# Kernel optimization log

Hardware: AMD Instinct MI355X
Metric: run time of the kernel (lower is better)

The kernel has to match this reference:

```python
import jax, jax.numpy as jnp
import numpy as np

BATCH, T, D_MODEL, DIM = 8, 4096, 512, 512
R_MIN, R_MAX, MAX_PHASE = 0.0, 1.0, 6.28


def setup_inputs() -> dict:
    key = jax.random.key(0)
    ks = jax.random.split(key, 8)
    x = jax.random.normal(ks[0], (BATCH, T, D_MODEL), dtype=jnp.float32)
    h0 = jnp.zeros((BATCH, 1, DIM), dtype=jnp.float32)
    # nu_log / theta_log per the module's initializers
    u1 = jax.random.uniform(ks[1], (DIM,))
    nu_log = jnp.log(-0.5 * jnp.log(u1 * (R_MAX ** 2 - R_MIN ** 2) + R_MIN ** 2)).astype(jnp.float32)
    u2 = jax.random.uniform(ks[2], (DIM,))
    theta_log = jnp.log(MAX_PHASE * u2).astype(jnp.float32)
    # B ~ N(0,1)/sqrt(2*D_in), C ~ N(0,1)/sqrt(D_out)
    B_re = (jax.random.normal(ks[3], (D_MODEL, DIM)) / jnp.sqrt(2.0 * D_MODEL)).astype(jnp.float32)
    B_im = (jax.random.normal(ks[4], (D_MODEL, DIM)) / jnp.sqrt(2.0 * D_MODEL)).astype(jnp.float32)
    C_re = (jax.random.normal(ks[5], (DIM, D_MODEL)) / jnp.sqrt(float(D_MODEL))).astype(jnp.float32)
    C_im = (jax.random.normal(ks[6], (DIM, D_MODEL)) / jnp.sqrt(float(D_MODEL))).astype(jnp.float32)
    D_param = jax.random.normal(ks[7], (D_MODEL,)).astype(jnp.float32)
    # gamma_log = log(sqrt(1 - |Lambda|^2)) with Lambda from nu/theta
    diag_lambda = jnp.exp(-jnp.exp(nu_log) + 1j * jnp.exp(theta_log))
    gamma_log = jnp.log(jnp.sqrt(1.0 - jnp.abs(diag_lambda) ** 2)).astype(jnp.float32)
    return {"x": x, "h0": h0, "nu_log": nu_log, "theta_log": theta_log,
            "B_re": B_re, "B_im": B_im, "C_re": C_re, "C_im": C_im,
            "D_param": D_param, "gamma_log": gamma_log}


def _binary_op(ei, ej):
    a_i, b_i = ei
    a_j, b_j = ej
    return (a_j * a_i, a_j * b_i + b_j)


def reference(x, h0, nu_log, theta_log, B_re, B_im, C_re, C_im, D_param, gamma_log):
    B, T_len, _ = x.shape
    Lambda = jnp.exp(-jnp.exp(nu_log) + 1j * jnp.exp(theta_log))            # (N,) complex
    B_norm = (B_re + 1j * B_im) * jnp.exp(gamma_log)[None, :]               # (D,N) complex
    C = C_re + 1j * C_im                                                     # (N,D) complex
    # Input projection: Bu[b,t,n] = sum_d x[b,t,d] * B_norm[d,n]
    Bu = jnp.einsum('btd,dn->btn', x.astype(jnp.complex64), B_norm)
    Bu = jnp.concatenate([h0.astype(jnp.complex64), Bu], axis=1)             # (B,T+1,N)
    Lam = jnp.broadcast_to(Lambda, Bu.shape)                                 # (B,T+1,N)
    _, H = jax.lax.associative_scan(_binary_op, (Lam, Bu), axis=1)
    H = H[:, 1:]                                                             # (B,T,N)
    y = jnp.einsum('btn,nd->btd', H, C).real + D_param * x                   # (B,T,D)
    new_h = H[:, -1:]                                                        # (B,1,N) complex
    return (y, new_h)
```

## Files before the change

kernel.cpp:

```cpp
#include <hip/hip_runtime.h>

#define T_LEN 4096
#define DMODEL 512
#define DIM 512
#define NBATCH 8
#define MROWS (NBATCH * T_LEN)
#define NCHUNK 128
#define LCHUNK 32

typedef __attribute__((ext_vector_type(8))) short short8;
typedef __attribute__((ext_vector_type(4))) float float4v;

__device__ __forceinline__ ushort f2b(float f) {
    union { float fl; unsigned u; } v; v.fl = f;
    unsigned u = v.u;
    return (ushort)((u + 0x7FFFu + ((u >> 16) & 1u)) >> 16);
}
__device__ __forceinline__ float b2f(ushort u) {
    union { unsigned u; float f; } v; v.u = (unsigned)u << 16; return v.f;
}

__device__ __forceinline__ void glds16(const ushort* g, ushort* l) {
    __builtin_amdgcn_global_load_lds(
        (const __attribute__((address_space(1))) void*)g,
        (__attribute__((address_space(3))) void*)l, 16, 0, 0);
}


__global__ __launch_bounds__(256) void k_prep_x(const float* __restrict__ x,
                                                ushort* __restrict__ xb) {
    int i = (blockIdx.x * 256 + threadIdx.x) * 4;
    float4 v = *(const float4*)(x + i);
    ushort4 o;
    o.x = f2b(v.x); o.y = f2b(v.y); o.z = f2b(v.z); o.w = f2b(v.w);
    *(ushort4*)(xb + i) = o;
}

__global__ __launch_bounds__(256) void k_prep_B(const float* __restrict__ Bre,
                                                const float* __restrict__ Bim,
                                                const float* __restrict__ gamma_log,
                                                ushort* __restrict__ BT) {
    int idx = blockIdx.x * 256 + threadIdx.x;
    int n = idx >> 9;
    int d = idx & 511;
    float v;
    if (n < 512) v = Bre[d * 512 + n] * __expf(gamma_log[n]);
    else { int nn = n - 512; v = Bim[d * 512 + nn] * __expf(gamma_log[nn]); }
    BT[idx] = f2b(v);
}

__global__ __launch_bounds__(256) void k_prep_C(const float* __restrict__ Cre,
                                                const float* __restrict__ Cim,
                                                ushort* __restrict__ CT) {
    int idx = blockIdx.x * 256 + threadIdx.x;
    int d = idx >> 10;
    int k = idx & 1023;
    float v = (k < 512) ? Cre[k * 512 + d] : -Cim[(k - 512) * 512 + d];
    CT[idx] = f2b(v);
}

template<int K, int MODE>
__global__ __launch_bounds__(256) void k_gemm(
    const ushort* __restrict__ A, const ushort* __restrict__ Bt,
    ushort* __restrict__ oRe, ushort* __restrict__ oIm,
    float* __restrict__ y, const float* __restrict__ x, const float* __restrict__ Dp) {
    __shared__ ushort sA[128 * 32];
    __shared__ ushort sB[128 * 32];
    const int tid = threadIdx.x;
    const int m0 = blockIdx.y * 128;
    const int n0 = blockIdx.x * 128;
    const int wave = tid >> 6;
    const int lane = tid & 63;
    const int wm = (wave >> 1) * 64;
    const int wn = (wave & 1) * 64;
    const int lr = lane & 15;
    const int quad = lane >> 4;

    const int srow = wave * 32 + (lane >> 2);
    const int scol = (lane & 3) * 8;
    const ushort* gA0 = A + (size_t)(m0 + srow) * K + scol;
    const ushort* gB0 = Bt + (size_t)(n0 + srow) * K + scol;
    ushort* lA0 = &sA[(wave * 32) * 32];
    ushort* lA1 = &sA[(wave * 32 + 16) * 32];
    ushort* lB0 = &sB[(wave * 32) * 32];
    ushort* lB1 = &sB[(wave * 32 + 16) * 32];

    float4v acc[4][4];
#pragma unroll
    for (int i = 0; i < 4; i++)
#pragma unroll
        for (int j = 0; j < 4; j++) {
            float4v z = {0.f, 0.f, 0.f, 0.f};
            acc[i][j] = z;
        }

    for (int k0 = 0; k0 < K; k0 += 32) {
        __syncthreads();
        glds16(gA0 + k0, lA0);
        glds16(gA0 + (size_t)16 * K + k0, lA1);
        glds16(gB0 + k0, lB0);
        glds16(gB0 + (size_t)16 * K + k0, lB1);
        __syncthreads();

        short8 af[4], bfr[4];
#pragma unroll
        for (int i = 0; i < 4; i++) af[i] = *(const short8*)&sA[(wm + i * 16 + lr) * 32 + quad * 8];
#pragma unroll
        for (int j = 0; j < 4; j++) bfr[j] = *(const short8*)&sB[(wn + j * 16 + lr) * 32 + quad * 8];
#pragma unroll
        for (int i = 0; i < 4; i++)
#pragma unroll
            for (int j = 0; j < 4; j++)
                acc[i][j] = __builtin_amdgcn_mfma_f32_16x16x32_bf16(af[i], bfr[j], acc[i][j], 0, 0, 0);
    }

#pragma unroll
    for (int i = 0; i < 4; i++) {
#pragma unroll
        for (int j = 0; j < 4; j++) {
            int gmb = m0 + wm + i * 16 + quad * 4;
            int gn = n0 + wn + j * 16 + lr;
#pragma unroll
            for (int r = 0; r < 4; r++) {
                float v = acc[i][j][r];
                int row = gmb + r;
                if (MODE == 1) {
                    if (gn < 512) oRe[(size_t)row * 512 + gn] = f2b(v);
                    else oIm[(size_t)row * 512 + (gn - 512)] = f2b(v);
                } else {
                    size_t o = (size_t)row * 512 + gn;
                    y[o] = v + Dp[gn] * x[o];
                }
            }
        }
    }
}


__device__ __forceinline__ void lambda_of(const float* nu_log, const float* theta_log,
                                          int n, float& lre, float& lim) {
    float e = __expf(nu_log[n]);
    float th = __expf(theta_log[n]);
    float rad = __expf(-e);
    float s, c;
    __sincosf(th, &s, &c);
    lre = rad * c;
    lim = rad * s;
}

__global__ __launch_bounds__(256) void k_scan1(const ushort* __restrict__ BuRe,
                                               const ushort* __restrict__ BuIm,
                                               const float* __restrict__ nu_log,
                                               const float* __restrict__ theta_log,
                                               float* __restrict__ cRe, float* __restrict__ cIm) {
    int n2 = threadIdx.x;
    int b = blockIdx.x >> 7;
    int c = blockIdx.x & 127;
    float lre0, lim0, lre1, lim1;
    lambda_of(nu_log, theta_log, 2 * n2, lre0, lim0);
    lambda_of(nu_log, theta_log, 2 * n2 + 1, lre1, lim1);
    float hr0 = 0.f, hi0 = 0.f, hr1 = 0.f, hi1 = 0.f;
    size_t base = ((size_t)b * T_LEN + (size_t)c * LCHUNK) * 512 + 2 * n2;
#pragma unroll 8
    for (int j = 0; j < LCHUNK; j++) {
        ushort2 ur = *(const ushort2*)(BuRe + base + (size_t)j * 512);
        ushort2 ui = *(const ushort2*)(BuIm + base + (size_t)j * 512);
        float br0 = b2f(ur.x), br1 = b2f(ur.y), bi0 = b2f(ui.x), bi1 = b2f(ui.y);
        float nr0 = lre0 * hr0 - lim0 * hi0 + br0;
        float ni0 = lre0 * hi0 + lim0 * hr0 + bi0;
        hr0 = nr0; hi0 = ni0;
        float nr1 = lre1 * hr1 - lim1 * hi1 + br1;
        float ni1 = lre1 * hi1 + lim1 * hr1 + bi1;
        hr1 = nr1; hi1 = ni1;
    }
    size_t co = ((size_t)b * NCHUNK + c) * 512 + 2 * n2;
    *(float2*)(cRe + co) = make_float2(hr0, hr1);
    *(float2*)(cIm + co) = make_float2(hi0, hi1);
}

__global__ __launch_bounds__(256) void k_scan2(const float* __restrict__ cRe,
                                               const float* __restrict__ cIm,
                                               const float* __restrict__ h0,
                                               const float* __restrict__ nu_log,
                                               const float* __restrict__ theta_log,
                                               float* __restrict__ pRe, float* __restrict__ pIm,
                                               float* __restrict__ newH, int newh_mode) {
    int idx = blockIdx.x * 256 + threadIdx.x;
    int b = idx >> 9;
    int n = idx & 511;
    float lre, lim;
    lambda_of(nu_log, theta_log, n, lre, lim);
    float Lr = lre, Li = lim;
#pragma unroll
    for (int s = 0; s < 5; s++) {
        float nr = Lr * Lr - Li * Li;
        float ni = 2.f * Lr * Li;
        Lr = nr; Li = ni;
    }
    float cr = h0[b * 512 + n];
    float ci = 0.f;
    for (int c = 0; c < NCHUNK; c++) {
        size_t o = ((size_t)b * NCHUNK + c) * 512 + n;
        pRe[o] = cr;
        pIm[o] = ci;
        float ar = cRe[o], ai = cIm[o];
        float nr = Lr * cr - Li * ci + ar;
        float ni = Lr * ci + Li * cr + ai;
        cr = nr; ci = ni;
    }
    size_t ci_idx = (size_t)b * 512 + n;
    if (newh_mode == 1) {
        newH[ci_idx] = cr;
        newH[(size_t)NBATCH * 512 + ci_idx] = ci;
    } else if (newh_mode == 2) {
        newH[ci_idx] = cr;
    } else {
        newH[ci_idx * 2] = cr;
        newH[ci_idx * 2 + 1] = ci;
    }
}

__global__ __launch_bounds__(256) void k_scan3(const ushort* __restrict__ BuRe,
                                               const ushort* __restrict__ BuIm,
                                               const float* __restrict__ pRe,
                                               const float* __restrict__ pIm,
                                               const float* __restrict__ nu_log,
                                               const float* __restrict__ theta_log,
                                               ushort* __restrict__ Hbf) {
    int n2 = threadIdx.x;
    int b = blockIdx.x >> 7;
    int c = blockIdx.x & 127;
    float lre0, lim0, lre1, lim1;
    lambda_of(nu_log, theta_log, 2 * n2, lre0, lim0);
    lambda_of(nu_log, theta_log, 2 * n2 + 1, lre1, lim1);
    size_t co = ((size_t)b * NCHUNK + c) * 512 + 2 * n2;
    float2 frv = *(const float2*)(pRe + co);
    float2 fiv = *(const float2*)(pIm + co);
    float fr0 = frv.x, fr1 = frv.y, fi0 = fiv.x, fi1 = fiv.y;
    float pr0 = lre0, pi0 = lim0, pr1 = lre1, pi1 = lim1;
    float hr0 = 0.f, hi0 = 0.f, hr1 = 0.f, hi1 = 0.f;
    size_t row0 = (size_t)b * T_LEN + (size_t)c * LCHUNK;
#pragma unroll 4
    for (int j = 0; j < LCHUNK; j++) {
        size_t base = (row0 + j) * 512 + 2 * n2;
        ushort2 ur = *(const ushort2*)(BuRe + base);
        ushort2 ui = *(const ushort2*)(BuIm + base);
        float br0 = b2f(ur.x), br1 = b2f(ur.y), bi0 = b2f(ui.x), bi1 = b2f(ui.y);
        float nr0 = lre0 * hr0 - lim0 * hi0 + br0;
        float ni0 = lre0 * hi0 + lim0 * hr0 + bi0;
        hr0 = nr0; hi0 = ni0;
        float nr1 = lre1 * hr1 - lim1 * hi1 + br1;
        float ni1 = lre1 * hi1 + lim1 * hr1 + bi1;
        hr1 = nr1; hi1 = ni1;
        float vr0 = hr0 + pr0 * fr0 - pi0 * fi0;
        float vi0 = hi0 + pr0 * fi0 + pi0 * fr0;
        float vr1 = hr1 + pr1 * fr1 - pi1 * fi1;
        float vi1 = hi1 + pr1 * fi1 + pi1 * fr1;
        size_t hrow = (row0 + j) * 1024;
        ushort2 wre, wim;
        wre.x = f2b(vr0); wre.y = f2b(vr1);
        wim.x = f2b(vi0); wim.y = f2b(vi1);
        *(ushort2*)(Hbf + hrow + 2 * n2) = wre;
        *(ushort2*)(Hbf + hrow + 512 + 2 * n2) = wim;
        float npr0 = pr0 * lre0 - pi0 * lim0;
        float npi0 = pr0 * lim0 + pi0 * lre0;
        pr0 = npr0; pi0 = npi0;
        float npr1 = pr1 * lre1 - pi1 * lim1;
        float npi1 = pr1 * lim1 + pi1 * lre1;
        pr1 = npr1; pi1 = npi1;
    }
}


extern "C" void kernel_launch(void* const* d_in, const int* in_sizes, int n_in,
                              void* d_out, int out_size, void* d_ws, size_t ws_size,
                              hipStream_t stream) {
    const float* x         = (const float*)d_in[0];
    const float* h0        = (const float*)d_in[1];
    const float* nu_log    = (const float*)d_in[2];
    const float* theta_log = (const float*)d_in[3];
    const float* B_re      = (const float*)d_in[4];
    const float* B_im      = (const float*)d_in[5];
    const float* C_re      = (const float*)d_in[6];
    const float* C_im      = (const float*)d_in[7];
    const float* D_param   = (const float*)d_in[8];
    const float* gamma_log = (const float*)d_in[9];

    char* ws = (char*)d_ws;
    size_t off = 0;
    ushort* Xb   = (ushort*)(ws + off); off += (size_t)MROWS * 512 * 2;
    ushort* BT   = (ushort*)(ws + off); off += (size_t)1024 * 512 * 2;
    ushort* CT   = (ushort*)(ws + off); off += (size_t)512 * 1024 * 2;
    ushort* BuRe = (ushort*)(ws + off); off += (size_t)MROWS * 512 * 2;
    ushort* BuIm = (ushort*)(ws + off); off += (size_t)MROWS * 512 * 2;
    ushort* Hbf  = (ushort*)(ws + off); off += (size_t)MROWS * 1024 * 2;
    float*  cRe  = (float*)(ws + off); off += (size_t)NBATCH * NCHUNK * 512 * 4;
    float*  cIm  = (float*)(ws + off); off += (size_t)NBATCH * NCHUNK * 512 * 4;
    float*  pRe  = (float*)(ws + off); off += (size_t)NBATCH * NCHUNK * 512 * 4;
    float*  pIm  = (float*)(ws + off); off += (size_t)NBATCH * NCHUNK * 512 * 4;

    float* y_out = (float*)d_out;
    float* newH  = (float*)d_out + (size_t)MROWS * 512;

    const int tail = out_size - MROWS * 512;
    int newh_mode = 0;
    if (tail == NBATCH * 512 * 2) newh_mode = 1;
    else if (tail == NBATCH * 512) newh_mode = 2;

    k_prep_x<<<dim3(MROWS * 512 / 4 / 256), dim3(256), 0, stream>>>(x, Xb);
    k_prep_B<<<dim3(1024 * 512 / 256), dim3(256), 0, stream>>>(B_re, B_im, gamma_log, BT);
    k_prep_C<<<dim3(512 * 1024 / 256), dim3(256), 0, stream>>>(C_re, C_im, CT);

    k_gemm<512, 1><<<dim3(1024 / 128, MROWS / 128), dim3(256), 0, stream>>>(
        Xb, BT, BuRe, BuIm, nullptr, nullptr, nullptr);

    k_scan1<<<dim3(NBATCH * NCHUNK), dim3(256), 0, stream>>>(BuRe, BuIm, nu_log, theta_log, cRe, cIm);
    k_scan2<<<dim3(NBATCH * 512 / 256), dim3(256), 0, stream>>>(cRe, cIm, h0, nu_log, theta_log, pRe, pIm, newH, newh_mode);
    k_scan3<<<dim3(NBATCH * NCHUNK), dim3(256), 0, stream>>>(BuRe, BuIm, pRe, pIm, nu_log, theta_log, Hbf);

    k_gemm<1024, 2><<<dim3(512 / 128, MROWS / 128), dim3(256), 0, stream>>>(
        Hbf, CT, nullptr, nullptr, y_out, x, D_param);
}
```

Baseline: 315.9 us.

## Deepen GEMM K tile with XOR-swizzled LDS, XCD-aware block mapping, smaller scan2 blocks

Both GEMMs now stage a 64-wide K slice per iteration, which halves the number of barrier pairs, and store it in LDS with an XOR swizzle to avoid bank conflicts. Blocks are launched on a 1D grid and remapped so that each XCD gets a contiguous band of M rows, which is meant to improve L2 reuse of the A tiles. The middle scan kernel uses 64-thread blocks so more CUs take part, and its chunk loop is unrolled. LDS use per block doubles, which may reduce occupancy.

Result: faster. 292.5 us (-7.4%).

```diff
diff --git a/kernel.cpp b/kernel.cpp
--- a/kernel.cpp
+++ b/kernel.cpp
@@ -59,16 +59,19 @@
     CT[idx] = f2b(v);
 }
 
-template<int K, int MODE>
+template<int K, int MODE, int NBN>
 __global__ __launch_bounds__(256) void k_gemm(
     const ushort* __restrict__ A, const ushort* __restrict__ Bt,
     ushort* __restrict__ oRe, ushort* __restrict__ oIm,
     float* __restrict__ y, const float* __restrict__ x, const float* __restrict__ Dp) {
-    __shared__ ushort sA[128 * 32];
-    __shared__ ushort sB[128 * 32];
+    __shared__ ushort sA[128 * 64];
+    __shared__ ushort sB[128 * 64];
     const int tid = threadIdx.x;
-    const int m0 = blockIdx.y * 128;
-    const int n0 = blockIdx.x * 128;
+    const int L = blockIdx.x;
+    const int xcd = L & 7;
+    const int slot = L >> 3;
+    const int m0 = (xcd * 32 + slot / NBN) * 128;
+    const int n0 = (slot % NBN) * 128;
     const int wave = tid >> 6;
     const int lane = tid & 63;
     const int wm = (wave >> 1) * 64;
@@ -76,14 +79,10 @@
     const int lr = lane & 15;
     const int quad = lane >> 4;
 
-    const int srow = wave * 32 + (lane >> 2);
-    const int scol = (lane & 3) * 8;
-    const ushort* gA0 = A + (size_t)(m0 + srow) * K + scol;
-    const ushort* gB0 = Bt + (size_t)(n0 + srow) * K + scol;
-    ushort* lA0 = &sA[(wave * 32) * 32];
-    ushort* lA1 = &sA[(wave * 32 + 16) * 32];
-    ushort* lB0 = &sB[(wave * 32) * 32];
-    ushort* lB1 = &sB[(wave * 32 + 16) * 32];
+    const int srow = lane >> 3;
+    const int schunk = (lane & 7) ^ srow;
+    const ushort* gA0 = A + (size_t)(m0 + wave * 32 + srow) * K + schunk * 8;
+    const ushort* gB0 = Bt + (size_t)(n0 + wave * 32 + srow) * K + schunk * 8;
 
     float4v acc[4][4];
 #pragma unroll
@@ -94,24 +93,34 @@
             acc[i][j] = z;
         }
 
-    for (int k0 = 0; k0 < K; k0 += 32) {
+    for (int k0 = 0; k0 < K; k0 += 64) {
         __syncthreads();
-        glds16(gA0 + k0, lA0);
-        glds16(gA0 + (size_t)16 * K + k0, lA1);
-        glds16(gB0 + k0, lB0);
-        glds16(gB0 + (size_t)16 * K + k0, lB1);
+#pragma unroll
+        for (int c = 0; c < 4; c++) {
+            glds16(gA0 + (size_t)(c * 8) * K + k0, &sA[(wave * 32 + c * 8) * 64]);
+            glds16(gB0 + (size_t)(c * 8) * K + k0, &sB[(wave * 32 + c * 8) * 64]);
+        }
         __syncthreads();
 
-        short8 af[4], bfr[4];
-#pragma unroll
-        for (int i = 0; i < 4; i++) af[i] = *(const short8*)&sA[(wm + i * 16 + lr) * 32 + quad * 8];
-#pragma unroll
-        for (int j = 0; j < 4; j++) bfr[j] = *(const short8*)&sB[(wn + j * 16 + lr) * 32 + quad * 8];
-#pragma unroll
-        for (int i = 0; i < 4; i++)
-#pragma unroll
-            for (int j = 0; j < 4; j++)
-                acc[i][j] = __builtin_amdgcn_mfma_f32_16x16x32_bf16(af[i], bfr[j], acc[i][j], 0, 0, 0);
+#pragma unroll
+        for (int kk = 0; kk < 2; kk++) {
+            short8 af[4], bfr[4];
+#pragma unroll
+            for (int i = 0; i < 4; i++) {
+                int row = wm + i * 16 + lr;
+                af[i] = *(const short8*)&sA[row * 64 + (((kk * 4 + quad) ^ (row & 7)) * 8)];
+            }
+#pragma unroll
+            for (int j = 0; j < 4; j++) {
+                int row = wn + j * 16 + lr;
+                bfr[j] = *(const short8*)&sB[row * 64 + (((kk * 4 + quad) ^ (row & 7)) * 8)];
+            }
+#pragma unroll
+            for (int i = 0; i < 4; i++)
+#pragma unroll
+                for (int j = 0; j < 4; j++)
+                    acc[i][j] = __builtin_amdgcn_mfma_f32_16x16x32_bf16(af[i], bfr[j], acc[i][j], 0, 0, 0);
+        }
     }
 
 #pragma unroll
@@ -178,14 +187,14 @@
     *(float2*)(cIm + co) = make_float2(hi0, hi1);
 }
 
-__global__ __launch_bounds__(256) void k_scan2(const float* __restrict__ cRe,
-                                               const float* __restrict__ cIm,
-                                               const float* __restrict__ h0,
-                                               const float* __restrict__ nu_log,
-                                               const float* __restrict__ theta_log,
-                                               float* __restrict__ pRe, float* __restrict__ pIm,
-                                               float* __restrict__ newH, int newh_mode) {
-    int idx = blockIdx.x * 256 + threadIdx.x;
+__global__ __launch_bounds__(64) void k_scan2(const float* __restrict__ cRe,
+                                              const float* __restrict__ cIm,
+                                              const float* __restrict__ h0,
+                                              const float* __restrict__ nu_log,
+                                              const float* __restrict__ theta_log,
+                                              float* __restrict__ pRe, float* __restrict__ pIm,
+                                              float* __restrict__ newH, int newh_mode) {
+    int idx = blockIdx.x * 64 + threadIdx.x;
     int b = idx >> 9;
     int n = idx & 511;
     float lre, lim;
@@ -199,6 +208,7 @@
     }
     float cr = h0[b * 512 + n];
     float ci = 0.f;
+#pragma unroll 4
     for (int c = 0; c < NCHUNK; c++) {
         size_t o = ((size_t)b * NCHUNK + c) * 512 + n;
         pRe[o] = cr;
@@ -311,13 +321,13 @@
     k_prep_B<<<dim3(1024 * 512 / 256), dim3(256), 0, stream>>>(B_re, B_im, gamma_log, BT);
     k_prep_C<<<dim3(512 * 1024 / 256), dim3(256), 0, stream>>>(C_re, C_im, CT);
 
-    k_gemm<512, 1><<<dim3(1024 / 128, MROWS / 128), dim3(256), 0, stream>>>(
+    k_gemm<512, 1, 8><<<dim3(2048), dim3(256), 0, stream>>>(
         Xb, BT, BuRe, BuIm, nullptr, nullptr, nullptr);
 
     k_scan1<<<dim3(NBATCH * NCHUNK), dim3(256), 0, stream>>>(BuRe, BuIm, nu_log, theta_log, cRe, cIm);
-    k_scan2<<<dim3(NBATCH * 512 / 256), dim3(256), 0, stream>>>(cRe, cIm, h0, nu_log, theta_log, pRe, pIm, newH, newh_mode);
+    k_scan2<<<dim3(NBATCH * 512 / 64), dim3(64), 0, stream>>>(cRe, cIm, h0, nu_log, theta_log, pRe, pIm, newH, newh_mode);
     k_scan3<<<dim3(NBATCH * NCHUNK), dim3(256), 0, stream>>>(BuRe, BuIm, pRe, pIm, nu_log, theta_log, Hbf);
 
-    k_gemm<1024, 2><<<dim3(512 / 128, MROWS / 128), dim3(256), 0, stream>>>(
+    k_gemm<1024, 2, 4><<<dim3(1024), dim3(256), 0, stream>>>(
         Hbf, CT, nullptr, nullptr, y_out, x, D_param);
 }
```
